# Kernel optimization log

Hardware: AMD Instinct MI355X
Metric: run time of the kernel (lower is better)

Reference implementation:

```python
import jax, jax.numpy as jnp
import numpy as np

V_SIZE = 32000
D = 1024
H = 16
HS = D // H          # 64
L = 4
T_BLOCK = 2048
B, T = 1, 2048
FF = 4 * D           # 4096
R_H = int(HS * 0.25)   # 16, per-head SVF rank
R_P = int(D * 0.25)    # 256, proj SVF rank
R_F = int(min(D, FF) * 0.25)  # 256, ffn SVF rank
STD = 0.02
EPS = 1e-5


def _ln(x, w, b):
    m = jnp.mean(x, axis=-1, keepdims=True)
    v = jnp.mean(jnp.square(x - m), axis=-1, keepdims=True)
    return (x - m) * jax.lax.rsqrt(v + EPS) * w + b


def _svf(x, Vw, z, Uw):
    # Vw: [r, in], z: [r], Uw: [out, r]  ->  ((x @ V^T) * z) @ U^T
    return ((x @ Vw.T) * z) @ Uw.T


def setup_inputs() -> dict:
    key = jax.random.key(0)
    ks = jax.random.split(key, 16)
    n = lambda k, shape: (jax.random.normal(k, shape, dtype=jnp.float32) * STD)
    inp = {
        "idx": jax.random.randint(ks[0], (B, T), 0, V_SIZE),
        "tok_emb": n(ks[1], (V_SIZE, D)),
        "pos_emb": n(ks[2], (T_BLOCK, D)),
        "ln1_w": jnp.ones((L, D)), "ln1_b": jnp.zeros((L, D)),
        "ln2_w": jnp.ones((L, D)), "ln2_b": jnp.zeros((L, D)),
        # kqv SVF factors stacked: axis0=layer, axis1=(k,q,v), axis2=head
        "kqv_V": n(ks[3], (L, 3, H, R_H, D)),
        "kqv_z": jnp.ones((L, 3, H, R_H)),
        "kqv_U": n(ks[4], (L, 3, H, HS, R_H)),
        "proj_V": n(ks[5], (L, R_P, D)),
        "proj_z": jnp.ones((L, R_P)),
        "proj_U": n(ks[6], (L, D, R_P)),
        "f1_V": n(ks[7], (L, R_F, D)),
        "f1_z": jnp.ones((L, R_F)),
        "f1_U": n(ks[8], (L, FF, R_F)),
        "f2_V": n(ks[9], (L, R_F, FF)),
        "f2_z": jnp.ones((L, R_F)),
        "f2_U": n(ks[10], (L, D, R_F)),
        "lnf_w": jnp.ones((D,)), "lnf_b": jnp.zeros((D,)),
        "lm_w": n(ks[11], (V_SIZE, D)),
    }
    return inp


def reference(idx, tok_emb, pos_emb, ln1_w, ln1_b, ln2_w, ln2_b,
              kqv_V, kqv_z, kqv_U, proj_V, proj_z, proj_U,
              f1_V, f1_z, f1_U, f2_V, f2_z, f2_U, lnf_w, lnf_b, lm_w):
    Bq, Tq = idx.shape
    x = tok_emb[idx] + pos_emb[:Tq]  # [B,T,D]
    causal = jnp.tril(jnp.ones((Tq, Tq), dtype=bool))
    for l in range(L):
        h = _ln(x, ln1_w[l], ln1_b[l])
        # per-head SVF: V projection, z scale, U projection (k,q,v in one einsum)
        t = jnp.einsum('btd,ghrd->gbthr', h, kqv_V[l]) * kqv_z[l][:, None, None]
        kqv = jnp.einsum('gbthr,ghsr->gbhts', t, kqv_U[l])  # [3,B,H,T,HS]
        k, q, v = kqv[0], kqv[1], kqv[2]
        wei = jnp.einsum('bhts,bhus->bhtu', q, k) * (HS ** -0.5)
        wei = jnp.where(causal, wei, -jnp.inf)
        wei = jax.nn.softmax(wei, axis=-1)
        att = jnp.einsum('bhtu,bhus->bhts', wei, v)           # [B,H,T,HS]
        att = att.transpose(0, 2, 1, 3).reshape(Bq, Tq, D)     # concat heads
        x = x + _svf(att, proj_V[l], proj_z[l], proj_U[l])
        h2 = _ln(x, ln2_w[l], ln2_b[l])
        ff = _svf(h2, f1_V[l], f1_z[l], f1_U[l])
        ff = jax.nn.gelu(ff, approximate=False)
        x = x + _svf(ff, f2_V[l], f2_z[l], f2_U[l])
    x = _ln(x, lnf_w, lnf_b)
    logits = x @ lm_w.T  # [B,T,vocab]
    return logits
```

## Files before the change

kernel.cpp:

```cpp
#include <hip/hip_runtime.h>
#include <hip/hip_bf16.h>


#define T_SEQ 2048
#define DMODEL 1024
#define NHEAD 16
#define HSZ 64
#define NLAYER 4
#define FFDIM 4096
#define RH 16
#define RP 256
#define RF 256
#define VOCAB 32000
#define NKQV (3 * NHEAD * RH)

typedef short short8 __attribute__((ext_vector_type(8)));
typedef float f32x4 __attribute__((ext_vector_type(4)));
typedef unsigned int uint_t;
typedef unsigned short ushort_t;

__device__ __forceinline__ float bfbits2f(uint_t bits16_in_low) {
    uint_t b = bits16_in_low << 16;
    float f;
    __builtin_memcpy(&f, &b, 4);
    return f;
}
__device__ __forceinline__ ushort_t f2bfu(float f) {
    union { __hip_bfloat16 b; ushort_t u; } cv;
    cv.b = __float2bfloat16(f);
    return cv.u;
}
__device__ __forceinline__ uint_t pack2bf(float a, float b) {
    return (uint_t)f2bfu(a) | ((uint_t)f2bfu(b) << 16);
}

__device__ __forceinline__ void gld16(const __hip_bfloat16* g, short* l) {
    __builtin_amdgcn_global_load_lds(
        (const __attribute__((address_space(1))) void*)g,
        (__attribute__((address_space(3))) void*)l, 16, 0, 0);
}

struct CvtArgs {
    const float* s[9];
    __hip_bfloat16* d[9];
    int n4[9];
};
__global__ __launch_bounds__(256) void cvtall_k(CvtArgs a, int total4) {
    int i = blockIdx.x * 256 + threadIdx.x;
    if (i >= total4) return;
#pragma unroll
    for (int k = 0; k < 9; ++k) {
        if (i < a.n4[k]) {
            float4 v = ((const float4*)a.s[k])[i];
            ushort4 o;
            o.x = f2bfu(v.x); o.y = f2bfu(v.y); o.z = f2bfu(v.z); o.w = f2bfu(v.w);
            ((ushort4*)a.d[k])[i] = o;
            return;
        }
        i -= a.n4[k];
    }
}

__global__ __launch_bounds__(256) void embed_k(const int* __restrict__ idx,
                                               const float* __restrict__ tok,
                                               const float* __restrict__ pos,
                                               float* __restrict__ x) {
    int i = blockIdx.x * 256 + threadIdx.x;
    int d4 = i & (DMODEL / 4 - 1);
    int t = i >> 8;
    int tk = idx[t];
    float4 a = ((const float4*)(tok + (size_t)tk * DMODEL))[d4];
    float4 p = ((const float4*)(pos + (size_t)t * DMODEL))[d4];
    a.x += p.x; a.y += p.y; a.z += p.z; a.w += p.w;
    ((float4*)(x + (size_t)t * DMODEL))[d4] = a;
}

__global__ __launch_bounds__(256) void ln_k(const float* __restrict__ xin,
                                            const float* __restrict__ w,
                                            const float* __restrict__ b,
                                            __hip_bfloat16* __restrict__ out) {
    const int row = blockIdx.x, tid = threadIdx.x;
    const float4 v = ((const float4*)(xin + (size_t)row * DMODEL))[tid];
    float s = v.x + v.y + v.z + v.w;
    float q = v.x * v.x + v.y * v.y + v.z * v.z + v.w * v.w;
    for (int off = 32; off; off >>= 1) { s += __shfl_xor(s, off); q += __shfl_xor(q, off); }
    __shared__ float rs_[4], rq_[4];
    if ((tid & 63) == 0) { rs_[tid >> 6] = s; rq_[tid >> 6] = q; }
    __syncthreads();
    s = rs_[0] + rs_[1] + rs_[2] + rs_[3];
    q = rq_[0] + rq_[1] + rq_[2] + rq_[3];
    const float mean = s * (1.f / DMODEL);
    const float var = q * (1.f / DMODEL) - mean * mean;
    const float rstd = rsqrtf(var + 1e-5f);
    const float4 wv = ((const float4*)w)[tid];
    const float4 bv = ((const float4*)b)[tid];
    ushort4 o;
    o.x = f2bfu((v.x - mean) * rstd * wv.x + bv.x);
    o.y = f2bfu((v.y - mean) * rstd * wv.y + bv.y);
    o.z = f2bfu((v.z - mean) * rstd * wv.z + bv.z);
    o.w = f2bfu((v.w - mean) * rstd * wv.w + bv.w);
    ((ushort4*)out)[(size_t)row * (DMODEL / 4) + tid] = o;
}

template <int BM, int BN, int MODE>
__global__ __launch_bounds__(256) void gemm_t(const __hip_bfloat16* __restrict__ A,
                                              const __hip_bfloat16* __restrict__ B,
                                              const float* __restrict__ colscale,
                                              __hip_bfloat16* __restrict__ Cb,
                                              float* __restrict__ Cf,
                                              int M, int N, int K) {
    constexpr int WM = (BN >= 128) ? 2 : 4;
    constexpr int WN = 4 / WM;
    constexpr int TM = BM / WM / 16;
    constexpr int TN = BN / WN / 16;
    constexpr int IA = BM / 32;
    constexpr int IB = BN / 32;
    __shared__ short As[BM * 64];
    __shared__ short Bs[BN * 64];
    const int tid = threadIdx.x;
    const int w = tid >> 6, ln = tid & 63, lr = ln & 15, lg = ln >> 4;
    const int GM = M / BM;

    const int nwg = gridDim.x;
    const int cpx = nwg >> 3;
    const int wg = (blockIdx.x & 7) * cpx + (blockIdx.x >> 3);
    const int bm = wg % GM, bn = wg / GM;
    const int wm = w / WN, wn = w % WN;

    f32x4 acc[TM][TN] = {};

    const int srow = tid >> 3;
    const int scol = (((tid & 7) ^ ((tid >> 3) & 7)) * 8);
    const __hip_bfloat16* Ag = A + (size_t)(bm * BM + srow) * K + scol;
    const __hip_bfloat16* Bg = B + (size_t)(bn * BN + srow) * K + scol;

    for (int kt = 0; kt < K; kt += 64) {
        __syncthreads();
#pragma unroll
        for (int i = 0; i < IA; ++i)
            gld16(Ag + (size_t)(i * 32) * K + kt, &As[i * 2048 + w * 512]);
#pragma unroll
        for (int i = 0; i < IB; ++i)
            gld16(Bg + (size_t)(i * 32) * K + kt, &Bs[i * 2048 + w * 512]);
        __syncthreads();

#pragma unroll
        for (int kk = 0; kk < 2; ++kk) {
            short8 af[TM], bf[TN];
#pragma unroll
            for (int m = 0; m < TM; ++m) {
                const int row = wm * (BM / WM) + m * 16 + lr;
                af[m] = *(const short8*)&As[row * 64 + (((kk * 4 + lg) ^ (lr & 7)) * 8)];
            }
#pragma unroll
            for (int n = 0; n < TN; ++n) {
                const int row = wn * (BN / WN) + n * 16 + lr;
                bf[n] = *(const short8*)&Bs[row * 64 + (((kk * 4 + lg) ^ (lr & 7)) * 8)];
            }
#pragma unroll
            for (int m = 0; m < TM; ++m)
#pragma unroll
                for (int n = 0; n < TN; ++n)
                    acc[m][n] = __builtin_amdgcn_mfma_f32_16x16x32_bf16(af[m], bf[n], acc[m][n], 0, 0, 0);
        }
    }

#pragma unroll
    for (int n = 0; n < TN; ++n) {
        const int col = bn * BN + wn * (BN / WN) + n * 16 + lr;
        float cs = 1.0f;
        if (MODE == 0 && colscale) cs = colscale[col];
#pragma unroll
        for (int m = 0; m < TM; ++m) {
#pragma unroll
            for (int rr = 0; rr < 4; ++rr) {
                const int row = bm * BM + wm * (BM / WM) + m * 16 + lg * 4 + rr;
                float v = acc[m][n][rr];
                const size_t o = (size_t)row * N + col;
                if (MODE == 0) {
                    Cb[o] = __float2bfloat16(v * cs);
                } else if (MODE == 1) {
                    v = 0.5f * v * (1.0f + erff(v * 0.70710678118654752f));
                    Cb[o] = __float2bfloat16(v);
                } else if (MODE == 2) {
                    Cf[o] += v;
                } else {
                    Cf[o] = v;
                }
            }
        }
    }
}

__global__ __launch_bounds__(256) void kqv2_k(const __hip_bfloat16* __restrict__ t1,
                                              const __hip_bfloat16* __restrict__ U,
                                              __hip_bfloat16* __restrict__ qb,
                                              __hip_bfloat16* __restrict__ kb2,
                                              __hip_bfloat16* __restrict__ vt2) {
    size_t i = (size_t)blockIdx.x * 256 + threadIdx.x;
    int s = (int)(i & 63);
    size_t rest = i >> 6;
    int t = (int)(rest & (T_SEQ - 1));
    int gh = (int)(rest >> 11);
    const short8* trow = (const short8*)(t1 + (size_t)t * NKQV + gh * RH);
    const short8* urow = (const short8*)(U + ((size_t)gh * HSZ + s) * RH);
    short8 ta = trow[0], tb = trow[1];
    short8 ua = urow[0], ub = urow[1];
    float acc = 0.f;
#pragma unroll
    for (int j = 0; j < 8; ++j) {
        acc += bfbits2f((ushort_t)ta[j]) * bfbits2f((ushort_t)ua[j]);
        acc += bfbits2f((ushort_t)tb[j]) * bfbits2f((ushort_t)ub[j]);
    }
    const ushort_t val = f2bfu(acc);
    const int g = gh >> 4, h = gh & 15;
    if (g == 1) {
        ((ushort_t*)qb)[((size_t)h * T_SEQ + t) * HSZ + s] = val;
    } else if (g == 0) {
        const int tile = t >> 6, gg = (t >> 4) & 3, lr = t & 15;
        const int half = s >> 5, lg = (s >> 3) & 3, j = s & 7;
        const int c = gg * 2 + half, ln = lg * 16 + lr;
        ((ushort_t*)kb2)[(((size_t)h * 32 + tile) * 8 + c) * 512 + ln * 8 + j] = val;
    } else {
        const int tile = t >> 6, half = (t >> 5) & 1, lg2 = (t >> 3) & 3, j2 = t & 7;
        const int dt = s >> 4, lr2 = s & 15;
        const int c = dt * 2 + half, ln = lg2 * 16 + lr2;
        ((ushort_t*)vt2)[(((size_t)h * 32 + tile) * 8 + c) * 512 + ln * 8 + j2] = val;
    }
}

__global__ __launch_bounds__(256) void attn_k(const __hip_bfloat16* __restrict__ qb,
                                              const __hip_bfloat16* __restrict__ kb2,
                                              const __hip_bfloat16* __restrict__ vt2,
                                              __hip_bfloat16* __restrict__ attout) {
    __shared__ short P_s[2][4][16 * 72];
    const int tid = threadIdx.x, w = tid >> 6, ln = tid & 63;
    const int lr = ln & 15, lg = ln >> 4;
    const int f = blockIdx.y * 32 + blockIdx.x;
    const int h = ((f & 7) << 1) | ((f >> 3) & 1);
    const int bi = f >> 4;
    const int t0 = bi * 16 + w * 512;
    const size_t hb = (size_t)h * T_SEQ;
    const size_t hB = (size_t)h * 32;
    const float SCL = 0.18033688011112042f;

    short8 qf0 = *(const short8*)(qb + (hb + t0 + lr) * HSZ + lg * 8);
    short8 qf1 = *(const short8*)(qb + (hb + t0 + lr) * HSZ + 32 + lg * 8);

    f32x4 acc[4] = {};
    float mrun = -3e38f, lrun = 0.f;
    int pbuf = 0;

    short8 kf[4][2];
#pragma unroll
    for (int g = 0; g < 4; ++g) {
        kf[g][0] = *(const short8*)(kb2 + (hB * 8 + g * 2 + 0) * 512 + (size_t)ln * 8);
        kf[g][1] = *(const short8*)(kb2 + (hB * 8 + g * 2 + 1) * 512 + (size_t)ln * 8);
    }

    for (int u0 = 0; u0 <= t0 + 15; u0 += 64) {
        const int it = u0 >> 6;
        f32x4 st[4];
#pragma unroll
        for (int g = 0; g < 4; ++g) {
            f32x4 z = {};
            z = __builtin_amdgcn_mfma_f32_16x16x32_bf16(kf[g][0], qf0, z, 0, 0, 0);
            st[g] = __builtin_amdgcn_mfma_f32_16x16x32_bf16(kf[g][1], qf1, z, 0, 0, 0);
        }

        const int un = u0 + 64;
        if (un <= t0 + 15) {
            const int itn = it + 1;
#pragma unroll
            for (int g = 0; g < 4; ++g) {
                kf[g][0] = *(const short8*)(kb2 + ((hB + itn) * 8 + g * 2 + 0) * 512 + (size_t)ln * 8);
                kf[g][1] = *(const short8*)(kb2 + ((hB + itn) * 8 + g * 2 + 1) * 512 + (size_t)ln * 8);
            }
        }
        short8 vf[4][2];
#pragma unroll
        for (int dt = 0; dt < 4; ++dt) {
            vf[dt][0] = *(const short8*)(vt2 + ((hB + it) * 8 + dt * 2 + 0) * 512 + (size_t)ln * 8);
            vf[dt][1] = *(const short8*)(vt2 + ((hB + it) * 8 + dt * 2 + 1) * 512 + (size_t)ln * 8);
        }

        const int qg = t0 + lr;
        float sv[16];
#pragma unroll
        for (int g = 0; g < 4; ++g) {
            const bool needm = (u0 + g * 16 + 15 > t0);
#pragma unroll
            for (int r = 0; r < 4; ++r) {
                float v = st[g][r] * SCL;
                if (needm && (u0 + g * 16 + lg * 4 + r > qg)) v = -1e30f;
                sv[g * 4 + r] = v;
            }
        }
        float tm = sv[0];
#pragma unroll
        for (int j = 1; j < 16; ++j) tm = fmaxf(tm, sv[j]);
        tm = fmaxf(tm, __shfl_xor(tm, 16));
        tm = fmaxf(tm, __shfl_xor(tm, 32));
        const float mnew = fmaxf(mrun, tm);
        const float corr = exp2f(mrun - mnew);
        float pv[16];
        float ls = 0.f;
#pragma unroll
        for (int j = 0; j < 16; ++j) { pv[j] = exp2f(sv[j] - mnew); ls += pv[j]; }
        ls += __shfl_xor(ls, 16);
        ls += __shfl_xor(ls, 32);
        lrun = lrun * corr + ls;
#pragma unroll
        for (int dt = 0; dt < 4; ++dt) acc[dt] *= corr;

        uint_t* pw = (uint_t*)P_s[pbuf][w];
        const int wb = lr * 36 + lg * 2;
#pragma unroll
        for (int g = 0; g < 4; ++g) {
            pw[wb + g * 8 + 0] = pack2bf(pv[g * 4 + 0], pv[g * 4 + 1]);
            pw[wb + g * 8 + 1] = pack2bf(pv[g * 4 + 2], pv[g * 4 + 3]);
        }
        asm volatile("s_waitcnt lgkmcnt(0)" ::: "memory");
        short8 pf0 = *(const short8*)(&P_s[pbuf][w][lr * 72 + lg * 8]);
        short8 pf1 = *(const short8*)(&P_s[pbuf][w][lr * 72 + 32 + lg * 8]);

#pragma unroll
        for (int dt = 0; dt < 4; ++dt) {
            acc[dt] = __builtin_amdgcn_mfma_f32_16x16x32_bf16(vf[dt][0], pf0, acc[dt], 0, 0, 0);
            acc[dt] = __builtin_amdgcn_mfma_f32_16x16x32_bf16(vf[dt][1], pf1, acc[dt], 0, 0, 0);
        }

        mrun = mnew;
        pbuf ^= 1;
    }

    const float inv = 1.f / lrun;
#pragma unroll
    for (int dt = 0; dt < 4; ++dt) {
#pragma unroll
        for (int r = 0; r < 4; r += 2) {
            uint_t pk = pack2bf(acc[dt][r] * inv, acc[dt][r + 1] * inv);
            *(uint_t*)(attout + (size_t)(t0 + lr) * DMODEL + h * HSZ + dt * 16 + lg * 4 + r) = pk;
        }
    }
}

extern "C" void kernel_launch(void* const* d_in, const int* in_sizes, int n_in,
                              void* d_out, int out_size, void* d_ws, size_t ws_size,
                              hipStream_t stream) {
    const int* idx = (const int*)d_in[0];
    const float* tok_emb = (const float*)d_in[1];
    const float* pos_emb = (const float*)d_in[2];
    const float* ln1_w = (const float*)d_in[3];
    const float* ln1_b = (const float*)d_in[4];
    const float* ln2_w = (const float*)d_in[5];
    const float* ln2_b = (const float*)d_in[6];
    const float* kqv_V = (const float*)d_in[7];
    const float* kqv_z = (const float*)d_in[8];
    const float* kqv_U = (const float*)d_in[9];
    const float* proj_V = (const float*)d_in[10];
    const float* proj_z = (const float*)d_in[11];
    const float* proj_U = (const float*)d_in[12];
    const float* f1_V = (const float*)d_in[13];
    const float* f1_z = (const float*)d_in[14];
    const float* f1_U = (const float*)d_in[15];
    const float* f2_V = (const float*)d_in[16];
    const float* f2_z = (const float*)d_in[17];
    const float* f2_U = (const float*)d_in[18];
    const float* lnf_w = (const float*)d_in[19];
    const float* lnf_b = (const float*)d_in[20];
    const float* lm_w = (const float*)d_in[21];

    char* W = (char*)d_ws;
    float* x = (float*)W;                 W += (size_t)T_SEQ * DMODEL * 4;
    __hip_bfloat16* hbuf = (__hip_bfloat16*)W; W += (size_t)T_SEQ * DMODEL * 2;
    __hip_bfloat16* t1 = (__hip_bfloat16*)W;   W += (size_t)T_SEQ * NKQV * 2;
    __hip_bfloat16* qbuf = (__hip_bfloat16*)W; W += (size_t)NHEAD * T_SEQ * HSZ * 2;
    __hip_bfloat16* kb2 = (__hip_bfloat16*)W;  W += (size_t)NHEAD * T_SEQ * HSZ * 2;
    __hip_bfloat16* vt2 = (__hip_bfloat16*)W;  W += (size_t)NHEAD * HSZ * T_SEQ * 2;
    __hip_bfloat16* attb = (__hip_bfloat16*)W; W += (size_t)T_SEQ * DMODEL * 2;
    __hip_bfloat16* ffb = (__hip_bfloat16*)W;  W += (size_t)T_SEQ * FFDIM * 2;
    __hip_bfloat16* wkV = (__hip_bfloat16*)W;  W += (size_t)NLAYER * NKQV * DMODEL * 2;
    __hip_bfloat16* wkU = (__hip_bfloat16*)W;  W += (size_t)NLAYER * 3 * NHEAD * HSZ * RH * 2;
    __hip_bfloat16* wpV = (__hip_bfloat16*)W;  W += (size_t)NLAYER * RP * DMODEL * 2;
    __hip_bfloat16* wpU = (__hip_bfloat16*)W;  W += (size_t)NLAYER * DMODEL * RP * 2;
    __hip_bfloat16* w1V = (__hip_bfloat16*)W;  W += (size_t)NLAYER * RF * DMODEL * 2;
    __hip_bfloat16* w1U = (__hip_bfloat16*)W;  W += (size_t)NLAYER * FFDIM * RF * 2;
    __hip_bfloat16* w2V = (__hip_bfloat16*)W;  W += (size_t)NLAYER * RF * FFDIM * 2;
    __hip_bfloat16* w2U = (__hip_bfloat16*)W;  W += (size_t)NLAYER * DMODEL * RF * 2;
    __hip_bfloat16* wlm = (__hip_bfloat16*)W;  W += (size_t)VOCAB * DMODEL * 2;

    {
        CvtArgs a;
        a.s[0] = kqv_V;  a.d[0] = wkV;  a.n4[0] = (int)((size_t)NLAYER * NKQV * DMODEL / 4);
        a.s[1] = kqv_U;  a.d[1] = wkU;  a.n4[1] = (int)((size_t)NLAYER * 3 * NHEAD * HSZ * RH / 4);
        a.s[2] = proj_V; a.d[2] = wpV;  a.n4[2] = (int)((size_t)NLAYER * RP * DMODEL / 4);
        a.s[3] = proj_U; a.d[3] = wpU;  a.n4[3] = (int)((size_t)NLAYER * DMODEL * RP / 4);
        a.s[4] = f1_V;   a.d[4] = w1V;  a.n4[4] = (int)((size_t)NLAYER * RF * DMODEL / 4);
        a.s[5] = f1_U;   a.d[5] = w1U;  a.n4[5] = (int)((size_t)NLAYER * FFDIM * RF / 4);
        a.s[6] = f2_V;   a.d[6] = w2V;  a.n4[6] = (int)((size_t)NLAYER * RF * FFDIM / 4);
        a.s[7] = f2_U;   a.d[7] = w2U;  a.n4[7] = (int)((size_t)NLAYER * DMODEL * RF / 4);
        a.s[8] = lm_w;   a.d[8] = wlm;  a.n4[8] = (int)((size_t)VOCAB * DMODEL / 4);
        int total4 = 0;
        for (int k = 0; k < 9; ++k) total4 += a.n4[k];
        cvtall_k<<<dim3((total4 + 255) / 256), dim3(256), 0, stream>>>(a, total4);
    }

    embed_k<<<dim3(T_SEQ * DMODEL / 4 / 256), dim3(256), 0, stream>>>(idx, tok_emb, pos_emb, x);

    const int M = T_SEQ;
    for (int l = 0; l < NLAYER; ++l) {
        ln_k<<<dim3(T_SEQ), dim3(256), 0, stream>>>(x, ln1_w + l * DMODEL, ln1_b + l * DMODEL, hbuf);
        gemm_t<64, 64, 0><<<dim3((M / 64) * (NKQV / 64)), dim3(256), 0, stream>>>(
            hbuf, wkV + (size_t)l * NKQV * DMODEL, kqv_z + (size_t)l * NKQV,
            t1, nullptr, M, NKQV, DMODEL);
        kqv2_k<<<dim3(3 * NHEAD * T_SEQ * HSZ / 256), dim3(256), 0, stream>>>(
            t1, wkU + (size_t)l * 3 * NHEAD * HSZ * RH, qbuf, kb2, vt2);
        attn_k<<<dim3(T_SEQ / 64, NHEAD), dim3(256), 0, stream>>>(qbuf, kb2, vt2, attb);
        gemm_t<64, 64, 0><<<dim3((M / 64) * (RP / 64)), dim3(256), 0, stream>>>(
            attb, wpV + (size_t)l * RP * DMODEL, proj_z + (size_t)l * RP,
            t1, nullptr, M, RP, DMODEL);
        gemm_t<128, 128, 2><<<dim3((M / 128) * (DMODEL / 128)), dim3(256), 0, stream>>>(
            t1, wpU + (size_t)l * DMODEL * RP, nullptr,
            nullptr, x, M, DMODEL, RP);
        ln_k<<<dim3(T_SEQ), dim3(256), 0, stream>>>(x, ln2_w + l * DMODEL, ln2_b + l * DMODEL, hbuf);
        gemm_t<64, 64, 0><<<dim3((M / 64) * (RF / 64)), dim3(256), 0, stream>>>(
            hbuf, w1V + (size_t)l * RF * DMODEL, f1_z + (size_t)l * RF,
            t1, nullptr, M, RF, DMODEL);
        gemm_t<128, 128, 1><<<dim3((M / 128) * (FFDIM / 128)), dim3(256), 0, stream>>>(
            t1, w1U + (size_t)l * FFDIM * RF, nullptr,
            ffb, nullptr, M, FFDIM, RF);
        gemm_t<64, 64, 0><<<dim3((M / 64) * (RF / 64)), dim3(256), 0, stream>>>(
            ffb, w2V + (size_t)l * RF * FFDIM, f2_z + (size_t)l * RF,
            t1, nullptr, M, RF, FFDIM);
        gemm_t<128, 128, 2><<<dim3((M / 128) * (DMODEL / 128)), dim3(256), 0, stream>>>(
            t1, w2U + (size_t)l * DMODEL * RF, nullptr,
            nullptr, x, M, DMODEL, RF);
    }
    ln_k<<<dim3(T_SEQ), dim3(256), 0, stream>>>(x, lnf_w, lnf_b, hbuf);
    gemm_t<128, 128, 3><<<dim3((M / 128) * (VOCAB / 128)), dim3(256), 0, stream>>>(
        hbuf, wlm, nullptr, nullptr, (float*)d_out, M, VOCAB, DMODEL);
}
```

Measured before the change: 1.177 ms.

## Add 256x256 double-buffered MFMA GEMM for LM head with XCD-aware block remap

Replaces the 128x128 generic GEMM for the vocab projection with a dedicated 256x256-tile kernel using 512 threads. It double-buffers LDS with direct global-to-LDS loads, uses XOR-swizzled addressing, and remaps workgroup IDs across the 8 XCDs to improve L2 locality. The larger tiles cut global traffic per FLOP on the largest GEMM, at the cost of heavy register and LDS use (128KB LDS, 128 accumulator VGPRs), which may limit occupancy. The grid size must divide evenly by 8 and M, N by 256; 32000/256 = 125, so the grid is 1000 blocks.

```diff
diff --git a/kernel.cpp b/kernel.cpp
--- a/kernel.cpp
+++ b/kernel.cpp
@@ -188,6 +188,102 @@
                     Cf[o] = v;
                 }
             }
+        }
+    }
+}
+
+__global__ __launch_bounds__(512, 2) void gemm256l(const __hip_bfloat16* __restrict__ A,
+                                                   const __hip_bfloat16* __restrict__ B,
+                                                   float* __restrict__ C,
+                                                   int M, int N, int K) {
+    __shared__ short As[2][256 * 64];
+    __shared__ short Bs[2][256 * 64];
+    const int tid = threadIdx.x;
+    const int w = tid >> 6, ln = tid & 63, lr = ln & 15, lg = ln >> 4;
+    const int wm = w >> 2, wn = w & 3;
+    const int GM = M / 256;
+
+    const int nwg = gridDim.x;
+    const int cpx = nwg >> 3;
+    const int wg = (blockIdx.x & 7) * cpx + (blockIdx.x >> 3);
+    const int bm = wg % GM, bn = wg / GM;
+
+    const int srow = tid >> 3;
+    const int scol = (((tid & 7) ^ ((tid >> 3) & 7)) * 8);
+    const __hip_bfloat16* Ag = A + (size_t)(bm * 256 + srow) * K + scol;
+    const __hip_bfloat16* Bg = B + (size_t)(bn * 256 + srow) * K + scol;
+    const int ldsb = w * 512;
+
+    f32x4 acc[8][4] = {};
+
+    auto STAGE = [&](int t) {
+        const int b = t & 1;
+        const size_t ko = (size_t)t * 64;
+#pragma unroll
+        for (int i = 0; i < 4; ++i) {
+            gld16(Ag + (size_t)(i * 64) * K + ko, &As[b][i * 4096 + ldsb]);
+            gld16(Bg + (size_t)(i * 64) * K + ko, &Bs[b][i * 4096 + ldsb]);
+        }
+    };
+
+    STAGE(0); STAGE(1);
+
+    const int T = K / 64;
+    for (int t = 0; t < T; ++t) {
+        if (t < T - 1) asm volatile("s_waitcnt vmcnt(8)" ::: "memory");
+        else           asm volatile("s_waitcnt vmcnt(0)" ::: "memory");
+        __builtin_amdgcn_s_barrier();
+
+        const short* Ab = As[t & 1];
+        const short* Bb = Bs[t & 1];
+        short8 af0[8], bf0[4], af1[8], bf1[4];
+#pragma unroll
+        for (int m = 0; m < 8; ++m) {
+            const int R = wm * 128 + m * 16 + lr;
+            af0[m] = *(const short8*)&Ab[R * 64 + ((lg ^ (lr & 7)) * 8)];
+        }
+#pragma unroll
+        for (int n = 0; n < 4; ++n) {
+            const int R = wn * 64 + n * 16 + lr;
+            bf0[n] = *(const short8*)&Bb[R * 64 + ((lg ^ (lr & 7)) * 8)];
+        }
+#pragma unroll
+        for (int m = 0; m < 8; ++m)
+#pragma unroll
+            for (int n = 0; n < 4; ++n)
+                acc[m][n] = __builtin_amdgcn_mfma_f32_16x16x32_bf16(af0[m], bf0[n], acc[m][n], 0, 0, 0);
+#pragma unroll
+        for (int m = 0; m < 8; ++m) {
+            const int R = wm * 128 + m * 16 + lr;
+            af1[m] = *(const short8*)&Ab[R * 64 + (((4 + lg) ^ (lr & 7)) * 8)];
+        }
+#pragma unroll
+        for (int n = 0; n < 4; ++n) {
+            const int R = wn * 64 + n * 16 + lr;
+            bf1[n] = *(const short8*)&Bb[R * 64 + (((4 + lg) ^ (lr & 7)) * 8)];
+        }
+        asm volatile("s_waitcnt lgkmcnt(0)" ::: "memory");
+        __builtin_amdgcn_s_barrier();
+        if (t + 2 < T) STAGE(t + 2);
+        __builtin_amdgcn_sched_barrier(0);
+        __builtin_amdgcn_s_setprio(1);
+#pragma unroll
+        for (int m = 0; m < 8; ++m)
+#pragma unroll
+            for (int n = 0; n < 4; ++n)
+                acc[m][n] = __builtin_amdgcn_mfma_f32_16x16x32_bf16(af1[m], bf1[n], acc[m][n], 0, 0, 0);
+        __builtin_amdgcn_s_setprio(0);
+    }
+
+#pragma unroll
+    for (int m = 0; m < 8; ++m) {
+        const int row = bm * 256 + wm * 128 + m * 16 + lg * 4;
+#pragma unroll
+        for (int rr = 0; rr < 4; ++rr) {
+            float* crow = C + (size_t)(row + rr) * N + bn * 256 + wn * 64 + lr;
+#pragma unroll
+            for (int n = 0; n < 4; ++n)
+                crow[n * 16] = acc[m][n][rr];
         }
     }
 }
@@ -438,6 +534,6 @@
             nullptr, x, M, DMODEL, RF);
     }
     ln_k<<<dim3(T_SEQ), dim3(256), 0, stream>>>(x, lnf_w, lnf_b, hbuf);
-    gemm_t<128, 128, 3><<<dim3((M / 128) * (VOCAB / 128)), dim3(256), 0, stream>>>(
-        hbuf, wlm, nullptr, nullptr, (float*)d_out, M, VOCAB, DMODEL);
-}
+    gemm256l<<<dim3((M / 256) * (VOCAB / 256)), dim3(512), 0, stream>>>(
+        hbuf, wlm, (float*)d_out, M, VOCAB, DMODEL);
+}
```

After: 1.161 ms. About the same (-1.4%).
